# Kernel optimization log

Measured on AMD Instinct MI355X. Metric: run time of the kernel, lower is better.

The kernel has to match this reference:

```python
import jax, jax.numpy as jnp
import numpy as np

GRID = 128          # voxel grid extent per axis
KERNELS = [2, 4, 8] # kernel_size == stride pooling scales
B = 4               # number of batches (point clouds)


def _pool_unpool(feats, seg, num_seg):
    # avg-pool over segment then broadcast back to original points
    sums = jax.ops.segment_sum(feats, seg, num_segments=num_seg)
    cnts = jax.ops.segment_sum(jnp.ones((feats.shape[0], 1), feats.dtype), seg, num_segments=num_seg)
    means = sums / jnp.maximum(cnts, 1.0)
    return means[seg]


def setup_inputs() -> dict:
    key = jax.random.key(0)
    k1, k2, k3, k4, k5 = jax.random.split(key, 5)
    N, C, OUT = 1_048_576, 64, 96
    mult = len(KERNELS) + 1
    feats = jax.random.normal(k1, (N, C), jnp.float32)
    coords = jax.random.randint(k2, (N, 3), 0, GRID, jnp.int32)
    batch_idx = jax.random.randint(k3, (N,), 0, B, jnp.int32)
    W = jax.random.normal(k4, (OUT, C * mult), jnp.float32) / np.sqrt(C * mult)
    b = jax.random.normal(k5, (OUT,), jnp.float32) * 0.01
    return {"feats": feats, "coords": coords, "batch_idx": batch_idx, "W": W, "b": b}


def reference(feats, coords, batch_idx, W, b):
    bidx = batch_idx.astype(jnp.int32)
    # i == 0: global average pooling per batch + MinkowskiBroadcast back to points
    cat = [_pool_unpool(feats, bidx, B)]
    # pyramid levels: AvgPool(k, stride=k) then PoolingTranspose(k, stride=k)
    for k in KERNELS:
        s = GRID // k  # pooled grid size per axis
        pc = coords // k
        seg = ((bidx * s + pc[:, 0]) * s + pc[:, 1]) * s + pc[:, 2]
        cat.append(_pool_unpool(feats, seg, B * s * s * s))
    out = jnp.concatenate(cat, axis=1)  # [N, C * (len(KERNELS)+1)]
    return out @ W.T + b                # MinkowskiLinear
```

## Files before the change

### kernel.cpp

```cpp
#include <hip/hip_runtime.h>
#include <stdint.h>


#define N_PTS   1048576
#define NB      4
#define N2SEG   (NB*64*64*64)
#define N4SEG   (NB*32*32*32)
#define N8SEG   (NB*16*16*16)

typedef unsigned int uint;

#define OFF_SUMS2  ((size_t)0)
#define OFF_CNT2   ((size_t)134217728)
#define OFF_SUMS0F ((size_t)138412032)
#define MEMSET_END ((size_t)138413056)
#define OFF_SUMS4  ((size_t)138413056)
#define OFF_MEAN4  ((size_t)155190272)
#define OFF_CNT4   ((size_t)171967488)
#define OFF_SUMS8  ((size_t)172491776)
#define OFF_MEAN8  ((size_t)174588928)
#define OFF_CNT8   ((size_t)176686080)
#define OFF_MEAN0  ((size_t)176751616)
#define OFF_WF     ((size_t)176752640)
#define WS_NEEDED  ((size_t)176801792)

typedef short s8v __attribute__((ext_vector_type(8)));
typedef float f4v __attribute__((ext_vector_type(4)));
typedef uint  u4v __attribute__((ext_vector_type(4)));

__device__ __forceinline__ uint pack_bf16x2(float a, float b) {
  uint ua = __float_as_uint(a), ub = __float_as_uint(b);
  ua = (ua + 0x7fffu + ((ua >> 16) & 1u)) >> 16;
  ub = (ub + 0x7fffu + ((ub >> 16) & 1u)) >> 16;
  return (ub << 16) | ua;
}
__device__ __forceinline__ float bflo(uint u) { return __uint_as_float(u << 16); }
__device__ __forceinline__ float bfhi(uint u) { return __uint_as_float(u & 0xffff0000u); }

__device__ __forceinline__ uint scale_pk(uint u, float rc) {
  return pack_bf16x2(bflo(u) * rc, bfhi(u) * rc);
}

#define ZERO_U4 (MEMSET_END / 16)
__global__ __launch_bounds__(256) void k_zero(u4v* __restrict__ p) {
  u4v z = (u4v)0u;
  size_t stride = (size_t)gridDim.x * 256;
  for (size_t i = blockIdx.x * 256ull + threadIdx.x; i < ZERO_U4; i += stride)
    __builtin_nontemporal_store(z, &p[i]);
}

__global__ __launch_bounds__(256) void k_wf(const float* __restrict__ W,
                                            uint* __restrict__ Wf) {
  int idx = blockIdx.x * 256 + threadIdx.x;
  int d = idx & 3, l = (idx >> 2) & 63, ktnt = idx >> 8;
  int kt = ktnt / 6, nt = ktnt - kt * 6;
  int n = nt * 16 + (l & 15);
  int k = kt * 32 + (l >> 4) * 8 + d * 2;
  Wf[idx] = pack_bf16x2(W[n * 256 + k], W[n * 256 + k + 1]);
}

__global__ __launch_bounds__(256) void k_scatter2(
    const float* __restrict__ feats, const int* __restrict__ coords,
    const int* __restrict__ batch, uint* __restrict__ sums2,
    uint* __restrict__ cnt2)
{
  int l = threadIdx.x & 63;
  int c2 = l & 31, half = l >> 5;
  int wid = (blockIdx.x * 256 + threadIdx.x) >> 6;
  int nw = (gridDim.x * 256) >> 6;
  for (int p0 = wid * 2; p0 < N_PTS; p0 += nw * 2) {
    int p = p0 + half;
    float2 f = ((const float2*)feats)[(size_t)p * 32 + c2];
    int b = batch[p];
    int x = coords[3 * p], y = coords[3 * p + 1], z = coords[3 * p + 2];
    int s2 = ((b * 64 + (x >> 1)) * 64 + (y >> 1)) * 64 + (z >> 1);
    uint pk = pack_bf16x2(f.x, f.y);
    uint64_t addr = (uint64_t)(uintptr_t)(sums2 + (size_t)s2 * 32 + c2);
    asm volatile("global_atomic_pk_add_bf16 %0, %1, off"
                 :: "v"(addr), "v"(pk) : "memory");
    if (c2 == 0) atomicAdd(&cnt2[s2], 1u);
  }
}

__global__ __launch_bounds__(256) void k_down_bf(
    const uint* __restrict__ sumsF, const uint* __restrict__ cntF,
    uint* __restrict__ sumsC, uint* __restrict__ meanC,
    uint* __restrict__ cntC, int lgC, int nC)
{
  int tid = blockIdx.x * 256 + threadIdx.x;
  int sc = tid >> 5, c2 = tid & 31;
  if (sc >= nC) return;
  int CG = 1 << lgC, FG = CG << 1;
  int b = sc >> (3 * lgC);
  int r = sc & ((1 << (3 * lgC)) - 1);
  int x = r >> (2 * lgC), y = (r >> lgC) & (CG - 1), z = r & (CG - 1);
  float sx = 0.f, sy = 0.f;
  uint cn = 0;
  #pragma unroll
  for (int dx = 0; dx < 2; ++dx)
    #pragma unroll
    for (int dy = 0; dy < 2; ++dy)
      #pragma unroll
      for (int dz = 0; dz < 2; ++dz) {
        int sf = ((b * FG + 2 * x + dx) * FG + (2 * y + dy)) * FG + (2 * z + dz);
        uint u = sumsF[(size_t)sf * 32 + c2];
        sx += bflo(u); sy += bfhi(u);
        cn += cntF[sf];
      }
  sumsC[(size_t)sc * 32 + c2] = pack_bf16x2(sx, sy);
  float rc = 1.0f / (float)(cn > 1u ? cn : 1u);
  meanC[(size_t)sc * 32 + c2] = pack_bf16x2(sx * rc, sy * rc);
  if (c2 == 0) cntC[sc] = cn;
}

__global__ __launch_bounds__(256) void k_gpart(
    const uint* __restrict__ sums8, float* __restrict__ sums0f)
{
  __shared__ float2 red[8][32];
  int b = blockIdx.x >> 5, chunk = blockIdx.x & 31;
  int t = threadIdx.x, c2 = t & 31, g = t >> 5;
  float sx = 0.f, sy = 0.f;
  for (int i = g; i < 128; i += 8) {
    uint u = sums8[(size_t)(b * 4096 + chunk * 128 + i) * 32 + c2];
    sx += bflo(u); sy += bfhi(u);
  }
  red[g][c2] = make_float2(sx, sy);
  __syncthreads();
  if (g == 0) {
    float ax = 0.f, ay = 0.f;
    #pragma unroll
    for (int i = 0; i < 8; ++i) { ax += red[i][c2].x; ay += red[i][c2].y; }
    unsafeAtomicAdd(&sums0f[b * 64 + 2 * c2], ax);
    unsafeAtomicAdd(&sums0f[b * 64 + 2 * c2 + 1], ay);
  }
}

__global__ __launch_bounds__(256) void k_fin0(
    const float* __restrict__ sums0f, const uint* __restrict__ cnt8,
    uint* __restrict__ mean0)
{
  __shared__ uint redc[256];
  __shared__ float rcs[NB];
  int t = threadIdx.x;
  uint cn = 0;
  for (int i = 0; i < 64; ++i) cn += cnt8[t * 64 + i];
  redc[t] = cn;
  __syncthreads();
  if (t < NB) {
    uint s = 0;
    for (int i = 0; i < 64; ++i) s += redc[t * 64 + i];
    rcs[t] = 1.0f / (float)(s > 1u ? s : 1u);
  }
  __syncthreads();
  if (t < 128) {
    int b = t >> 5, c2 = t & 31;
    float rc = rcs[b];
    mean0[b * 32 + c2] =
        pack_bf16x2(sums0f[b * 64 + 2 * c2] * rc, sums0f[b * 64 + 2 * c2 + 1] * rc);
  }
}

#define GPB 8
__global__ __launch_bounds__(256) void k_final(
    const int* __restrict__ coords, const int* __restrict__ batch,
    const uint* __restrict__ mean0,
    const uint* __restrict__ sums2, const uint* __restrict__ cnt2,
    const uint* __restrict__ mean4, const uint* __restrict__ mean8,
    const uint4* __restrict__ Wf, const float* __restrict__ bias,
    float* __restrict__ out)
{
  __shared__ uint4 wf[3072];
  int t = threadIdx.x;
  #pragma unroll
  for (int i = 0; i < 12; ++i) wf[i * 256 + t] = Wf[i * 256 + t];
  __syncthreads();
  int l = t & 63, w = t >> 6, pl = l & 15, q = l >> 4;
  #pragma unroll 1
  for (int g = 0; g < GPB; ++g) {
    int pbase = (blockIdx.x * GPB + g) * 64 + w * 16;
    int p = pbase + pl;
    int b = batch[p];
    int x = coords[3 * p], y = coords[3 * p + 1], z = coords[3 * p + 2];
    int s2 = ((b * 64 + (x >> 1)) * 64 + (y >> 1)) * 64 + (z >> 1);
    int s4 = ((b * 32 + (x >> 2)) * 32 + (y >> 2)) * 32 + (z >> 2);
    int s8 = ((b * 16 + (x >> 3)) * 16 + (y >> 3)) * 16 + (z >> 3);
    const uint4* r0 = (const uint4*)(mean0 + (size_t)b * 32);
    const uint4* r2 = (const uint4*)(sums2 + (size_t)s2 * 32);
    const uint4* r4 = (const uint4*)(mean4 + (size_t)s4 * 32);
    const uint4* r8 = (const uint4*)(mean8 + (size_t)s8 * 32);
    uint4 af[8];
    af[0] = r0[q];     af[1] = r0[4 + q];
    af[2] = r2[q];     af[3] = r2[4 + q];
    af[4] = r4[q];     af[5] = r4[4 + q];
    af[6] = r8[q];     af[7] = r8[4 + q];
    uint cv = cnt2[s2];
    float rc = 1.0f / (float)(cv > 1u ? cv : 1u);
    af[2].x = scale_pk(af[2].x, rc); af[2].y = scale_pk(af[2].y, rc);
    af[2].z = scale_pk(af[2].z, rc); af[2].w = scale_pk(af[2].w, rc);
    af[3].x = scale_pk(af[3].x, rc); af[3].y = scale_pk(af[3].y, rc);
    af[3].z = scale_pk(af[3].z, rc); af[3].w = scale_pk(af[3].w, rc);
    f4v acc[6];
    #pragma unroll
    for (int nt = 0; nt < 6; ++nt) acc[nt] = (f4v)0.0f;
    #pragma unroll
    for (int kt = 0; kt < 8; ++kt) {
      s8v afr = __builtin_bit_cast(s8v, af[kt]);
      #pragma unroll
      for (int nt = 0; nt < 6; ++nt) {
        s8v bf = __builtin_bit_cast(s8v, wf[(kt * 6 + nt) * 64 + l]);
        acc[nt] = __builtin_amdgcn_mfma_f32_16x16x32_bf16(afr, bf, acc[nt], 0, 0, 0);
      }
    }
    #pragma unroll
    for (int nt = 0; nt < 6; ++nt) {
      float bn = bias[nt * 16 + pl];
      #pragma unroll
      for (int r = 0; r < 4; ++r)
        out[(size_t)(pbase + q * 4 + r) * 96 + nt * 16 + pl] = bn + acc[nt][r];
    }
  }
}

extern "C" void kernel_launch(void* const* d_in, const int* in_sizes, int n_in,
                              void* d_out, int out_size, void* d_ws, size_t ws_size,
                              hipStream_t stream)
{
  const float* feats  = (const float*)d_in[0];
  const int*   coords = (const int*)d_in[1];
  const int*   batch  = (const int*)d_in[2];
  const float* W      = (const float*)d_in[3];
  const float* bias   = (const float*)d_in[4];
  float* out = (float*)d_out;
  char* ws = (char*)d_ws;
  if (ws_size < WS_NEEDED) return;

  uint*  sums2  = (uint*)(ws + OFF_SUMS2);
  uint*  cnt2   = (uint*)(ws + OFF_CNT2);
  float* sums0f = (float*)(ws + OFF_SUMS0F);
  uint*  sums4  = (uint*)(ws + OFF_SUMS4);
  uint*  mean4  = (uint*)(ws + OFF_MEAN4);
  uint*  cnt4   = (uint*)(ws + OFF_CNT4);
  uint*  sums8  = (uint*)(ws + OFF_SUMS8);
  uint*  mean8  = (uint*)(ws + OFF_MEAN8);
  uint*  cnt8   = (uint*)(ws + OFF_CNT8);
  uint*  mean0  = (uint*)(ws + OFF_MEAN0);
  uint*  Wf     = (uint*)(ws + OFF_WF);

  k_zero<<<2048, 256, 0, stream>>>((u4v*)ws);
  k_wf<<<48, 256, 0, stream>>>(W, Wf);
  k_scatter2<<<8192, 256, 0, stream>>>(feats, coords, batch, sums2, cnt2);
  k_down_bf<<<(N4SEG * 32) / 256, 256, 0, stream>>>(sums2, cnt2, sums4, mean4, cnt4, 5, N4SEG);
  k_down_bf<<<(N8SEG * 32) / 256, 256, 0, stream>>>(sums4, cnt4, sums8, mean8, cnt8, 4, N8SEG);
  k_gpart<<<128, 256, 0, stream>>>(sums8, sums0f);
  k_fin0<<<1, 256, 0, stream>>>(sums0f, cnt8, mean0);
  k_final<<<N_PTS / (GPB * 64), 256, 0, stream>>>(
      coords, batch, mean0, sums2, cnt2, mean4, mean8,
      (const uint4*)Wf, bias, out);
}
```

Before: 461.6 us.

## Software-pipeline gather loads in final GEMM kernel and use 32-bit workspace offsets

The final kernel now prefetches the next group's coordinates and pooled feature rows into registers while the current group's MFMA work runs, hiding gather latency. The weight copy into shared memory now overlaps the bias load because the barrier moved. All pooled buffers are reached through one workspace base pointer with 32-bit offsets, which cuts 64-bit address arithmetic, and the bias values are hoisted out of the loop. The memory clobber is also dropped from the bf16 atomic asm. The cost is about doubled register use for the prefetched rows, which may lower occupancy.

```diff
diff --git a/kernel.cpp b/kernel.cpp
--- a/kernel.cpp
+++ b/kernel.cpp
@@ -24,6 +24,12 @@
 #define OFF_WF     ((size_t)176752640)
 #define WS_NEEDED  ((size_t)176801792)
 
+#define D_S2 0u
+#define D_C2 ((uint)(OFF_CNT2 / 4))
+#define D_M4 ((uint)(OFF_MEAN4 / 4))
+#define D_M8 ((uint)(OFF_MEAN8 / 4))
+#define D_M0 ((uint)(OFF_MEAN0 / 4))
+
 typedef short s8v __attribute__((ext_vector_type(8)));
 typedef float f4v __attribute__((ext_vector_type(4)));
 typedef uint  u4v __attribute__((ext_vector_type(4)));
@@ -77,7 +83,7 @@
     uint pk = pack_bf16x2(f.x, f.y);
     uint64_t addr = (uint64_t)(uintptr_t)(sums2 + (size_t)s2 * 32 + c2);
     asm volatile("global_atomic_pk_add_bf16 %0, %1, off"
-                 :: "v"(addr), "v"(pk) : "memory");
+                 :: "v"(addr), "v"(pk));
     if (c2 == 0) atomicAdd(&cnt2[s2], 1u);
   }
 }
@@ -163,9 +169,7 @@
 #define GPB 8
 __global__ __launch_bounds__(256) void k_final(
     const int* __restrict__ coords, const int* __restrict__ batch,
-    const uint* __restrict__ mean0,
-    const uint* __restrict__ sums2, const uint* __restrict__ cnt2,
-    const uint* __restrict__ mean4, const uint* __restrict__ mean8,
+    const uint* __restrict__ wsb,
     const uint4* __restrict__ Wf, const float* __restrict__ bias,
     float* __restrict__ out)
 {
@@ -173,51 +177,82 @@
   int t = threadIdx.x;
   #pragma unroll
   for (int i = 0; i < 12; ++i) wf[i * 256 + t] = Wf[i * 256 + t];
-  __syncthreads();
   int l = t & 63, w = t >> 6, pl = l & 15, q = l >> 4;
-  #pragma unroll 1
-  for (int g = 0; g < GPB; ++g) {
-    int pbase = (blockIdx.x * GPB + g) * 64 + w * 16;
-    int p = pbase + pl;
+  float bn[6];
+  #pragma unroll
+  for (int nt = 0; nt < 6; ++nt) bn[nt] = bias[nt * 16 + pl];
+  __syncthreads();
+
+  uint4 afc[8];
+  uint cvc;
+  {
+    int p = blockIdx.x * (GPB * 64) + w * 16 + pl;
     int b = batch[p];
     int x = coords[3 * p], y = coords[3 * p + 1], z = coords[3 * p + 2];
     int s2 = ((b * 64 + (x >> 1)) * 64 + (y >> 1)) * 64 + (z >> 1);
     int s4 = ((b * 32 + (x >> 2)) * 32 + (y >> 2)) * 32 + (z >> 2);
     int s8 = ((b * 16 + (x >> 3)) * 16 + (y >> 3)) * 16 + (z >> 3);
-    const uint4* r0 = (const uint4*)(mean0 + (size_t)b * 32);
-    const uint4* r2 = (const uint4*)(sums2 + (size_t)s2 * 32);
-    const uint4* r4 = (const uint4*)(mean4 + (size_t)s4 * 32);
-    const uint4* r8 = (const uint4*)(mean8 + (size_t)s8 * 32);
-    uint4 af[8];
-    af[0] = r0[q];     af[1] = r0[4 + q];
-    af[2] = r2[q];     af[3] = r2[4 + q];
-    af[4] = r4[q];     af[5] = r4[4 + q];
-    af[6] = r8[q];     af[7] = r8[4 + q];
-    uint cv = cnt2[s2];
-    float rc = 1.0f / (float)(cv > 1u ? cv : 1u);
-    af[2].x = scale_pk(af[2].x, rc); af[2].y = scale_pk(af[2].y, rc);
-    af[2].z = scale_pk(af[2].z, rc); af[2].w = scale_pk(af[2].w, rc);
-    af[3].x = scale_pk(af[3].x, rc); af[3].y = scale_pk(af[3].y, rc);
-    af[3].z = scale_pk(af[3].z, rc); af[3].w = scale_pk(af[3].w, rc);
+    const uint4* a0 = (const uint4*)(wsb + D_M0 + b * 32);
+    const uint4* a2 = (const uint4*)(wsb + D_S2 + s2 * 32);
+    const uint4* a4 = (const uint4*)(wsb + D_M4 + s4 * 32);
+    const uint4* a8 = (const uint4*)(wsb + D_M8 + s8 * 32);
+    afc[0] = a0[q];     afc[1] = a0[4 + q];
+    afc[2] = a2[q];     afc[3] = a2[4 + q];
+    afc[4] = a4[q];     afc[5] = a4[4 + q];
+    afc[6] = a8[q];     afc[7] = a8[4 + q];
+    cvc = wsb[D_C2 + s2];
+  }
+
+  #pragma unroll 1
+  for (int g = 0; g < GPB; ++g) {
+    uint4 afn[8];
+    uint cvn = 0;
+    if (g + 1 < GPB) {
+      int p = blockIdx.x * (GPB * 64) + (g + 1) * 64 + w * 16 + pl;
+      int b = batch[p];
+      int x = coords[3 * p], y = coords[3 * p + 1], z = coords[3 * p + 2];
+      int s2 = ((b * 64 + (x >> 1)) * 64 + (y >> 1)) * 64 + (z >> 1);
+      int s4 = ((b * 32 + (x >> 2)) * 32 + (y >> 2)) * 32 + (z >> 2);
+      int s8 = ((b * 16 + (x >> 3)) * 16 + (y >> 3)) * 16 + (z >> 3);
+      const uint4* a0 = (const uint4*)(wsb + D_M0 + b * 32);
+      const uint4* a2 = (const uint4*)(wsb + D_S2 + s2 * 32);
+      const uint4* a4 = (const uint4*)(wsb + D_M4 + s4 * 32);
+      const uint4* a8 = (const uint4*)(wsb + D_M8 + s8 * 32);
+      afn[0] = a0[q];     afn[1] = a0[4 + q];
+      afn[2] = a2[q];     afn[3] = a2[4 + q];
+      afn[4] = a4[q];     afn[5] = a4[4 + q];
+      afn[6] = a8[q];     afn[7] = a8[4 + q];
+      cvn = wsb[D_C2 + s2];
+    }
+
+    float rc = 1.0f / (float)(cvc > 1u ? cvc : 1u);
+    afc[2].x = scale_pk(afc[2].x, rc); afc[2].y = scale_pk(afc[2].y, rc);
+    afc[2].z = scale_pk(afc[2].z, rc); afc[2].w = scale_pk(afc[2].w, rc);
+    afc[3].x = scale_pk(afc[3].x, rc); afc[3].y = scale_pk(afc[3].y, rc);
+    afc[3].z = scale_pk(afc[3].z, rc); afc[3].w = scale_pk(afc[3].w, rc);
     f4v acc[6];
     #pragma unroll
     for (int nt = 0; nt < 6; ++nt) acc[nt] = (f4v)0.0f;
     #pragma unroll
     for (int kt = 0; kt < 8; ++kt) {
-      s8v afr = __builtin_bit_cast(s8v, af[kt]);
+      s8v afr = __builtin_bit_cast(s8v, afc[kt]);
       #pragma unroll
       for (int nt = 0; nt < 6; ++nt) {
         s8v bf = __builtin_bit_cast(s8v, wf[(kt * 6 + nt) * 64 + l]);
         acc[nt] = __builtin_amdgcn_mfma_f32_16x16x32_bf16(afr, bf, acc[nt], 0, 0, 0);
       }
     }
-    #pragma unroll
-    for (int nt = 0; nt < 6; ++nt) {
-      float bn = bias[nt * 16 + pl];
+    int pbase = blockIdx.x * (GPB * 64) + g * 64 + w * 16;
+    float* ob = out + (size_t)(pbase + q * 4) * 96 + pl;
+    #pragma unroll
+    for (int nt = 0; nt < 6; ++nt)
       #pragma unroll
       for (int r = 0; r < 4; ++r)
-        out[(size_t)(pbase + q * 4 + r) * 96 + nt * 16 + pl] = bn + acc[nt][r];
-    }
+        ob[r * 96 + nt * 16] = bn[nt] + acc[nt][r];
+
+    #pragma unroll
+    for (int i = 0; i < 8; ++i) afc[i] = afn[i];
+    cvc = cvn;
   }
 }
 
@@ -254,6 +289,5 @@
   k_gpart<<<128, 256, 0, stream>>>(sums8, sums0f);
   k_fin0<<<1, 256, 0, stream>>>(sums0f, cnt8, mean0);
   k_final<<<N_PTS / (GPB * 64), 256, 0, stream>>>(
-      coords, batch, mean0, sums2, cnt2, mean4, mean8,
-      (const uint4*)Wf, bias, out);
-}
+      coords, batch, (const uint*)ws, (const uint4*)Wf, bias, out);
+}
```

Measured after the change: 428.2 us. 1.08x faster.
